# Kernel tuning notes

Hardware: AMD Instinct MI355X
Metric: run time of the kernel (lower is better)

Reference implementation:

```python
import jax, jax.numpy as jnp
import numpy as np

T, HID = 2048, 2048
H, KV, D = 16, 2, 256
ROT = 64  # head_dim * partial_rotary_factor (0.25)
THETA = 1.0e7
EPS = 1e-6
SCALE = D ** -0.5


def setup_inputs() -> dict:
    key = jax.random.key(0)
    ks = jax.random.split(key, 6)
    return {
        "positions": jnp.arange(T, dtype=jnp.int64 if jax.config.jax_enable_x64 else jnp.int32),
        "hidden_states": jax.random.normal(ks[0], (T, HID), jnp.float32),
        "wq": jax.random.normal(ks[1], (H * D * 2, HID), jnp.float32) * 0.02,
        "wk": jax.random.normal(ks[2], (KV * D, HID), jnp.float32) * 0.02,
        "wv": jax.random.normal(ks[3], (KV * D, HID), jnp.float32) * 0.02,
        "wo": jax.random.normal(ks[4], (HID, H * D), jnp.float32) * 0.02,
        "q_norm_w": jnp.zeros((D,), jnp.float32),
        "k_norm_w": jnp.zeros((D,), jnp.float32),
    }


def _rmsnorm(x, w):
    xf = x.astype(jnp.float32)
    out = xf * jax.lax.rsqrt(jnp.mean(xf * xf, axis=-1, keepdims=True) + EPS)
    return (out * (1.0 + w.astype(jnp.float32))).astype(x.dtype)


def _rope(positions, x):
    # partial rotary: first ROT dims, neox (rotate-half) style
    inv_freq = 1.0 / (THETA ** (jnp.arange(0, ROT, 2, dtype=jnp.float32) / ROT))
    freqs = positions.astype(jnp.float32)[:, None] * inv_freq  # [T, ROT/2]
    cos = jnp.cos(freqs)[:, None, :]  # [T,1,ROT/2]
    sin = jnp.sin(freqs)[:, None, :]
    x1 = x[..., : ROT // 2]
    x2 = x[..., ROT // 2 : ROT]
    rot = jnp.concatenate([x1 * cos - x2 * sin, x2 * cos + x1 * sin], axis=-1)
    return jnp.concatenate([rot, x[..., ROT:]], axis=-1)


def reference(positions, hidden_states, wq, wk, wv, wo, q_norm_w, k_norm_w):
    t = hidden_states.shape[0]
    q_out = (hidden_states @ wq.T).reshape(t, H, 2 * D)
    query, gate = q_out[..., :D], q_out[..., D:]
    gate = gate.reshape(t, H * D)
    k = (hidden_states @ wk.T).reshape(t, KV, D)
    v = (hidden_states @ wv.T).reshape(t, KV, D)

    query = _rmsnorm(query, q_norm_w)
    k = _rmsnorm(k, k_norm_w)
    query = _rope(positions, query)
    k = _rope(positions, k)

    # GQA: expand KV heads to H heads
    rep = H // KV
    k = jnp.repeat(k, rep, axis=1)  # [t, H, D]
    v = jnp.repeat(v, rep, axis=1)

    scores = jnp.einsum("qhd,khd->hqk", query, k) * SCALE
    causal = jnp.tril(jnp.ones((t, t), dtype=bool))
    scores = jnp.where(causal[None], scores, jnp.finfo(scores.dtype).min)
    probs = jax.nn.softmax(scores, axis=-1)
    o = jnp.einsum("hqk,khd->qhd", probs, v).reshape(t, H * D)

    o = o * jax.nn.sigmoid(gate)
    return o @ wo.T
```

## Files before the change

### kernel.cpp

```cpp
#include <hip/hip_runtime.h>
#include <hip/hip_bf16.h>

#define T_LEN 2048
#define HID_DIM 2048
#define NH 16
#define NKV 2
#define HD 256
#define ROT 64
#define EPS_F 1e-6f
#define SCALE_F 0.0625f
#define THETA_F 10000000.0f

typedef __bf16 bf16x8 __attribute__((ext_vector_type(8)));
typedef float floatx4 __attribute__((ext_vector_type(4)));

__device__ __forceinline__ unsigned short f2bf(float x) {
  unsigned int u = __float_as_uint(x);
  unsigned int rounding = 0x7FFFu + ((u >> 16) & 1u);
  return (unsigned short)((u + rounding) >> 16);
}
__device__ __forceinline__ float bf2f(unsigned short u) {
  return __uint_as_float(((unsigned int)u) << 16);
}
__device__ __forceinline__ floatx4 mfma16(bf16x8 a, bf16x8 b, floatx4 c) {
  return __builtin_amdgcn_mfma_f32_16x16x32_bf16(a, b, c, 0, 0, 0);
}
__device__ __forceinline__ void gl_lds16(const unsigned short* g, unsigned short* l) {
  __builtin_amdgcn_global_load_lds(
      (const __attribute__((address_space(1))) unsigned int*)g,
      (__attribute__((address_space(3))) unsigned int*)l, 16, 0, 0);
}

__global__ __launch_bounds__(256) void cvt_all(
    const float* __restrict__ hs, const float* __restrict__ wq,
    const float* __restrict__ wk, const float* __restrict__ wv,
    const float* __restrict__ wo, unsigned short* __restrict__ hsb,
    unsigned short* __restrict__ qkvwb, unsigned short* __restrict__ wob,
    const int* __restrict__ pos, float2* __restrict__ tab) {
  int i = blockIdx.x * 256 + threadIdx.x;
  if (i >= 7864320) {
    const int tid = i - 7864320;
    const int t = tid >> 5, fi = tid & 31;
    const float fr = (float)pos[t] * exp2f(-(float)fi * (23.2534966642f / 32.0f));
    tab[tid] = make_float2(cosf(fr), sinf(fr));
    return;
  }
  const float4* s4;
  ushort4* d4;
  int j;
  if (i < 1048576) { s4 = (const float4*)hs; d4 = (ushort4*)hsb; j = i; }
  else if (i < 5242880) { s4 = (const float4*)wq; d4 = (ushort4*)qkvwb; j = i - 1048576; }
  else if (i < 5505024) { s4 = (const float4*)wk; d4 = (ushort4*)qkvwb + 4194304; j = i - 5242880; }
  else if (i < 5767168) { s4 = (const float4*)wv; d4 = (ushort4*)qkvwb + 4456448; j = i - 5505024; }
  else { s4 = (const float4*)wo; d4 = (ushort4*)wob; j = i - 5767168; }
  float4 v = s4[j];
  ushort4 o;
  o.x = f2bf(v.x); o.y = f2bf(v.y); o.z = f2bf(v.z); o.w = f2bf(v.w);
  d4[j] = o;
}

__global__ __launch_bounds__(256) void gemm_bf16_bt(
    const unsigned short* __restrict__ A,
    const unsigned short* __restrict__ B,
    void* __restrict__ Cv, void* __restrict__ Cv2, int M, int N, int ld,
    int Ksub, int c_bf16, unsigned short* __restrict__ vTout) {
  __shared__ alignas(16) unsigned short As[2][128 * 32];
  __shared__ alignas(16) unsigned short Bs[2][128 * 32];
  const int tid = threadIdx.x;
  const int m0 = blockIdx.y * 128;
  const int n0 = blockIdx.x * 128;
  const int koff = blockIdx.z * Ksub;
  const int lane = tid & 63;
  const int wave = tid >> 6;
  const int wm = (wave >> 1) * 64;
  const int wn = (wave & 1) * 64;
  const int lrow = lane & 15;
  const int kgrp = lane >> 4;

  const unsigned short* aG = A + (size_t)(m0 + wave * 32 + (lane >> 2)) * ld + (lane & 3) * 8 + koff;
  const unsigned short* bG = B + (size_t)(n0 + wave * 32 + (lane >> 2)) * ld + (lane & 3) * 8 + koff;

  auto stage = [&](int k0, int b) {
    gl_lds16(aG + k0, &As[b][(wave * 32) * 32]);
    gl_lds16(aG + (size_t)16 * ld + k0, &As[b][(wave * 32 + 16) * 32]);
    gl_lds16(bG + k0, &Bs[b][(wave * 32) * 32]);
    gl_lds16(bG + (size_t)16 * ld + k0, &Bs[b][(wave * 32 + 16) * 32]);
  };

  floatx4 acc[4][4];
#pragma unroll
  for (int i = 0; i < 4; i++)
#pragma unroll
    for (int j = 0; j < 4; j++) acc[i][j] = floatx4{0.f, 0.f, 0.f, 0.f};

  stage(0, 0);
  __syncthreads();
  int cur = 0;
  for (int k0 = 0; k0 < Ksub; k0 += 32) {
    if (k0 + 32 < Ksub) stage(k0 + 32, cur ^ 1);
    bf16x8 af[4], bfr[4];
#pragma unroll
    for (int i = 0; i < 4; i++)
      af[i] = *reinterpret_cast<const bf16x8*>(&As[cur][(wm + i * 16 + lrow) * 32 + kgrp * 8]);
#pragma unroll
    for (int j = 0; j < 4; j++)
      bfr[j] = *reinterpret_cast<const bf16x8*>(&Bs[cur][(wn + j * 16 + lrow) * 32 + kgrp * 8]);
#pragma unroll
    for (int i = 0; i < 4; i++)
#pragma unroll
      for (int j = 0; j < 4; j++)
        acc[i][j] = mfma16(af[i], bfr[j], acc[i][j]);
    __syncthreads();
    cur ^= 1;
  }

  if (c_bf16) {
    unsigned short* C = (unsigned short*)Cv;
    const bool vtile = (vTout != nullptr) && (n0 >= 8704);
#pragma unroll
    for (int i = 0; i < 4; i++) {
      int row = m0 + wm + i * 16 + kgrp * 4;
#pragma unroll
      for (int j = 0; j < 4; j++) {
        int col = n0 + wn + j * 16 + lrow;
        if (vtile) {
          unsigned short* vrow = vTout + (size_t)(col - 8704) * T_LEN + row;
#pragma unroll
          for (int r = 0; r < 4; r++) vrow[r] = f2bf(acc[i][j][r]);
        } else {
#pragma unroll
          for (int r = 0; r < 4; r++)
            C[(size_t)(row + r) * N + col] = f2bf(acc[i][j][r]);
        }
      }
    }
  } else {
    float* base = (blockIdx.z < 2) ? (float*)Cv : (float*)Cv2;
    float* C = base + (size_t)(blockIdx.z & 1) * M * N;
#pragma unroll
    for (int i = 0; i < 4; i++) {
      int row = m0 + wm + i * 16 + kgrp * 4;
#pragma unroll
      for (int j = 0; j < 4; j++) {
        int col = n0 + wn + j * 16 + lrow;
#pragma unroll
        for (int r = 0; r < 4; r++)
          C[(size_t)(row + r) * N + col] = acc[i][j][r];
      }
    }
  }
}

__global__ __launch_bounds__(256) void add_out(
    const float* __restrict__ p0, const float* __restrict__ p1,
    float* __restrict__ out, int n4) {
  int i = blockIdx.x * 256 + threadIdx.x;
  if (i >= n4) return;
  float4 a = ((const float4*)p0)[i];
  float4 b = ((const float4*)p0)[i + n4];
  float4 c = ((const float4*)p1)[i];
  float4 d = ((const float4*)p1)[i + n4];
  float4 o;
  o.x = (a.x + b.x) + (c.x + d.x);
  o.y = (a.y + b.y) + (c.y + d.y);
  o.z = (a.z + b.z) + (c.z + d.z);
  o.w = (a.w + b.w) + (c.w + d.w);
  ((float4*)out)[i] = o;
}

__global__ __launch_bounds__(256) void norm_rope_fused(
    const unsigned short* __restrict__ qkv, const float* __restrict__ qw,
    const float* __restrict__ kw, const float2* __restrict__ tab,
    unsigned short* __restrict__ qbf, unsigned short* __restrict__ kbf) {
  const int t = blockIdx.x;
  const int y = blockIdx.y;
  const int wv = threadIdx.x >> 6;
  const int lane = threadIdx.x & 63;
  const unsigned short* in;
  const float* w;
  unsigned short* outp;
  if (y < 4) {
    const int h = y * 4 + wv;
    in = qkv + (size_t)t * 9216 + h * 512;
    w = qw;
    outp = qbf + (size_t)t * (NH * HD) + h * HD;
  } else {
    if (wv >= NKV) return;
    in = qkv + (size_t)t * 9216 + 8192 + wv * HD;
    w = kw;
    outp = kbf + (size_t)t * (NKV * HD) + wv * HD;
  }
  const int d0 = lane * 4;
  ushort4 v = *reinterpret_cast<const ushort4*>(in + d0);
  float x0 = bf2f(v.x), x1 = bf2f(v.y), x2 = bf2f(v.z), x3 = bf2f(v.w);
  float ss = (x0 * x0 + x1 * x1) + (x2 * x2 + x3 * x3);
#pragma unroll
  for (int m = 32; m >= 1; m >>= 1) ss += __shfl_xor(ss, m);
  const float rms = rsqrtf(ss * (1.0f / 256.0f) + EPS_F);
  float4 w4 = *reinterpret_cast<const float4*>(w + d0);
  float y0 = x0 * rms * (1.0f + w4.x);
  float y1 = x1 * rms * (1.0f + w4.y);
  float y2 = x2 * rms * (1.0f + w4.z);
  float y3 = x3 * rms * (1.0f + w4.w);
  if (lane < 16) {
    float p0 = __shfl_xor(y0, 8);
    float p1 = __shfl_xor(y1, 8);
    float p2 = __shfl_xor(y2, 8);
    float p3 = __shfl_xor(y3, 8);
    const float2* trow = tab + t * 32 + (d0 & 31);
    float4 cs01 = *reinterpret_cast<const float4*>(trow);
    float4 cs23 = *reinterpret_cast<const float4*>(trow + 2);
    if (d0 < 32) {
      y0 = y0 * cs01.x - p0 * cs01.y;
      y1 = y1 * cs01.z - p1 * cs01.w;
      y2 = y2 * cs23.x - p2 * cs23.y;
      y3 = y3 * cs23.z - p3 * cs23.w;
    } else {
      y0 = p0 * cs01.y + y0 * cs01.x;
      y1 = p1 * cs01.w + y1 * cs01.z;
      y2 = p2 * cs23.y + y2 * cs23.x;
      y3 = p3 * cs23.w + y3 * cs23.z;
    }
  }
  ushort4 ov;
  ov.x = f2bf(y0); ov.y = f2bf(y1); ov.z = f2bf(y2); ov.w = f2bf(y3);
  *reinterpret_cast<ushort4*>(outp + d0) = ov;
}

__global__ __launch_bounds__(256, 2) void attn_fwd(
    const unsigned short* __restrict__ qbf,
    const unsigned short* __restrict__ kbf,
    const unsigned short* __restrict__ vT,
    const unsigned short* __restrict__ qkvout,
    unsigned short* __restrict__ og)
{
  const int t = 31 - (int)blockIdx.x;
  const int h = blockIdx.y;
  const int wv = threadIdx.x >> 6;
  const int lane = threadIdx.x & 63;
  const int lrow = lane & 15;
  const int kgrp = lane >> 4;
  const int kv = h >> 3;
  const int q0 = t * 64 + wv * 16;
  const int nb = t * 2 + 2;

  __shared__ alignas(16) unsigned short Ks[32 * 256];
  __shared__ alignas(16) unsigned short Vs[2][256 * 32];
  __shared__ alignas(16) unsigned short Ps[4][16 * 32];

  auto stage_k = [&](int kb) {
#pragma unroll
    for (int i = 0; i < 4; ++i) {
      const int inst = wv * 4 + i;
      const int key_loc = inst * 2 + (lane >> 5);
      const int c = (lane & 31) ^ (key_loc & 7);
      const unsigned short* g =
          kbf + (size_t)(kb + key_loc) * (NKV * HD) + kv * HD + c * 8;
      gl_lds16(g, &Ks[inst * 512]);
    }
  };
  auto stage_v = [&](int kb, int buf) {
#pragma unroll
    for (int i = 0; i < 4; ++i) {
      const int inst = wv * 4 + i;
      const int dim = inst * 16 + (lane >> 2);
      const int c = (lane & 3) ^ (dim & 3);
      const unsigned short* g =
          vT + (size_t)(kv * HD + dim) * T_LEN + kb + c * 8;
      gl_lds16(g, &Vs[buf][inst * 512]);
    }
  };

  bf16x8 qa[8];
  {
    const unsigned short* qr = qbf + (size_t)(q0 + lrow) * (NH * HD) + h * HD + kgrp * 8;
#pragma unroll
    for (int s = 0; s < 8; s++)
      qa[s] = *reinterpret_cast<const bf16x8*>(qr + s * 32);
  }

  float lp[4] = {0.f, 0.f, 0.f, 0.f};
  floatx4 o[16];
#pragma unroll
  for (int dt = 0; dt < 16; dt++) o[dt] = floatx4{0.f, 0.f, 0.f, 0.f};

  stage_k(0);
  stage_v(0, 0);

  for (int ib = 0; ib < nb; ++ib) {
    const int kb = ib * 32;
    __syncthreads();
    if (ib + 1 < nb) stage_v(kb + 32, (ib + 1) & 1);

    const bool d = kb <= q0 + 15;

    floatx4 s0[2];
#pragma unroll
    for (int j = 0; j < 2; j++) s0[j] = floatx4{0.f, 0.f, 0.f, 0.f};
#pragma unroll
    for (int j = 0; j < 2; ++j) {
      const int ks = kb + j * 16;
      if (!(d && (ks <= q0 + 15))) continue;
      bf16x8 kf[8];
#pragma unroll
      for (int s = 0; s < 8; s++)
        kf[s] = *reinterpret_cast<const bf16x8*>(
            &Ks[(j * 16 + lrow) * 256 + (((s * 4 + kgrp) ^ (lrow & 7)) * 8)]);
#pragma unroll
      for (int s = 0; s < 8; s++) s0[j] = mfma16(qa[s], kf[s], s0[j]);
    }

    if (d) {
#pragma unroll
      for (int r = 0; r < 4; ++r) {
        const int qr = q0 + kgrp * 4 + r;
        float p0 = (kb + lrow <= qr) ? __expf(s0[0][r] * SCALE_F) : 0.f;
        float p1 = (kb + 16 + lrow <= qr) ? __expf(s0[1][r] * SCALE_F) : 0.f;
        lp[r] += p0 + p1;
        Ps[wv][(kgrp * 4 + r) * 32 + lrow] = f2bf(p0);
        Ps[wv][(kgrp * 4 + r) * 32 + 16 + lrow] = f2bf(p1);
      }
    }

    __syncthreads();
    if (ib + 1 < nb) stage_k(kb + 32);

    if (d) {
      bf16x8 pa = *reinterpret_cast<const bf16x8*>(&Ps[wv][lrow * 32 + kgrp * 8]);
      const unsigned short* vsb = &Vs[ib & 1][0];
#pragma unroll
      for (int dt = 0; dt < 16; ++dt) {
        const int dd = dt * 16 + lrow;
        bf16x8 bv = *reinterpret_cast<const bf16x8*>(
            &vsb[dd * 32 + ((kgrp ^ (lrow & 3)) * 8)]);
        o[dt] = mfma16(pa, bv, o[dt]);
      }
    }
  }

#pragma unroll
  for (int r = 0; r < 4; ++r) {
#pragma unroll
    for (int m = 8; m >= 1; m >>= 1) lp[r] += __shfl_xor(lp[r], m);
  }

#pragma unroll
  for (int r = 0; r < 4; ++r) {
    const int row = q0 + kgrp * 4 + r;
    const float inv_l = 1.0f / lp[r];
    const unsigned short* grow = qkvout + (size_t)row * 9216 + h * 512 + 256;
    unsigned short* orow = og + (size_t)row * (NH * HD) + h * HD;
#pragma unroll
    for (int dt = 0; dt < 16; dt++) {
      int dim = dt * 16 + lrow;
      float g = bf2f(grow[dim]);
      float val = o[dt][r] * inv_l;
      val *= 1.0f / (1.0f + __expf(-g));
      orow[dim] = f2bf(val);
    }
  }
}

extern "C" void kernel_launch(void* const* d_in, const int* in_sizes, int n_in,
                              void* d_out, int out_size, void* d_ws, size_t ws_size,
                              hipStream_t stream) {
  const int* positions = (const int*)d_in[0];
  const float* hidden = (const float*)d_in[1];
  const float* wq = (const float*)d_in[2];
  const float* wk = (const float*)d_in[3];
  const float* wv = (const float*)d_in[4];
  const float* wo = (const float*)d_in[5];
  const float* qnw = (const float*)d_in[6];
  const float* knw = (const float*)d_in[7];
  float* out = (float*)d_out;

  char* ws = (char*)d_ws;
  size_t off = 0;
  auto alloc = [&](size_t elems) -> unsigned short* {
    unsigned short* p = (unsigned short*)(ws + off);
    off += (elems * 2 + 255) & ~(size_t)255;
    return p;
  };
  unsigned short* hsb    = alloc((size_t)T_LEN * HID_DIM);
  unsigned short* qkvwb  = alloc((size_t)9216 * HID_DIM);
  unsigned short* wob    = alloc((size_t)HID_DIM * NH * HD);
  unsigned short* qkvout = alloc((size_t)T_LEN * 9216);
  unsigned short* qbf    = alloc((size_t)T_LEN * NH * HD);
  unsigned short* kbf    = alloc((size_t)T_LEN * NKV * HD);
  unsigned short* vTb    = alloc((size_t)NKV * HD * T_LEN);
  unsigned short* og     = alloc((size_t)T_LEN * NH * HD);
  float2* ropetab = (float2*)alloc((size_t)T_LEN * 32 * 4);
  float* part01 = (float*)ws;
  float* part23 = (float*)qkvout;

  cvt_all<<<30976, 256, 0, stream>>>(hidden, wq, wk, wv, wo, hsb, qkvwb, wob,
                                     positions, ropetab);

  gemm_bf16_bt<<<dim3(72, 16, 1), 256, 0, stream>>>(hsb, qkvwb, qkvout, nullptr,
                                                    2048, 9216, 2048, 2048, 1, vTb);

  norm_rope_fused<<<dim3(T_LEN, 5), 256, 0, stream>>>(qkvout, qnw, knw, ropetab, qbf, kbf);

  attn_fwd<<<dim3(32, NH), 256, 0, stream>>>(qbf, kbf, vTb, qkvout, og);

  gemm_bf16_bt<<<dim3(16, 16, 4), 256, 0, stream>>>(og, wob, part01, part23,
                                                    2048, 2048, 4096, 1024, 0, nullptr);
  add_out<<<4096, 256, 0, stream>>>(part01, part23, out, 1048576);
}
```

Measured before the change: 439.7 us.

## Fuse Q norm and RoPE into attention prologue and halve output split-K

Query RMSNorm and partial RoPE are now applied inside the attention kernel directly from the QKV GEMM output, so the separate q buffer write/read disappears and the norm kernel only handles K. The output projection uses split-K of 2 instead of 4, shrinking the partial-sum traffic and simplifying the final reduction. K/V staging is issued before the Q prologue to overlap its latency. The trade-off is extra per-thread ALU work in attention and fewer blocks in the output GEMM.

```diff
diff --git a/kernel.cpp b/kernel.cpp
--- a/kernel.cpp
+++ b/kernel.cpp
@@ -152,44 +152,24 @@
 }
 
 __global__ __launch_bounds__(256) void add_out(
-    const float* __restrict__ p0, const float* __restrict__ p1,
-    float* __restrict__ out, int n4) {
+    const float* __restrict__ p, float* __restrict__ out, int n4) {
   int i = blockIdx.x * 256 + threadIdx.x;
   if (i >= n4) return;
-  float4 a = ((const float4*)p0)[i];
-  float4 b = ((const float4*)p0)[i + n4];
-  float4 c = ((const float4*)p1)[i];
-  float4 d = ((const float4*)p1)[i + n4];
+  float4 a = ((const float4*)p)[i];
+  float4 b = ((const float4*)p)[i + n4];
   float4 o;
-  o.x = (a.x + b.x) + (c.x + d.x);
-  o.y = (a.y + b.y) + (c.y + d.y);
-  o.z = (a.z + b.z) + (c.z + d.z);
-  o.w = (a.w + b.w) + (c.w + d.w);
+  o.x = a.x + b.x; o.y = a.y + b.y; o.z = a.z + b.z; o.w = a.w + b.w;
   ((float4*)out)[i] = o;
 }
 
-__global__ __launch_bounds__(256) void norm_rope_fused(
-    const unsigned short* __restrict__ qkv, const float* __restrict__ qw,
-    const float* __restrict__ kw, const float2* __restrict__ tab,
-    unsigned short* __restrict__ qbf, unsigned short* __restrict__ kbf) {
+__global__ __launch_bounds__(128) void norm_rope_k(
+    const unsigned short* __restrict__ qkv, const float* __restrict__ kw,
+    const float2* __restrict__ tab, unsigned short* __restrict__ kbf) {
   const int t = blockIdx.x;
-  const int y = blockIdx.y;
   const int wv = threadIdx.x >> 6;
   const int lane = threadIdx.x & 63;
-  const unsigned short* in;
-  const float* w;
-  unsigned short* outp;
-  if (y < 4) {
-    const int h = y * 4 + wv;
-    in = qkv + (size_t)t * 9216 + h * 512;
-    w = qw;
-    outp = qbf + (size_t)t * (NH * HD) + h * HD;
-  } else {
-    if (wv >= NKV) return;
-    in = qkv + (size_t)t * 9216 + 8192 + wv * HD;
-    w = kw;
-    outp = kbf + (size_t)t * (NKV * HD) + wv * HD;
-  }
+  const unsigned short* in = qkv + (size_t)t * 9216 + 8192 + wv * HD;
+  unsigned short* outp = kbf + (size_t)t * (NKV * HD) + wv * HD;
   const int d0 = lane * 4;
   ushort4 v = *reinterpret_cast<const ushort4*>(in + d0);
   float x0 = bf2f(v.x), x1 = bf2f(v.y), x2 = bf2f(v.z), x3 = bf2f(v.w);
@@ -197,7 +177,7 @@
 #pragma unroll
   for (int m = 32; m >= 1; m >>= 1) ss += __shfl_xor(ss, m);
   const float rms = rsqrtf(ss * (1.0f / 256.0f) + EPS_F);
-  float4 w4 = *reinterpret_cast<const float4*>(w + d0);
+  float4 w4 = *reinterpret_cast<const float4*>(kw + d0);
   float y0 = x0 * rms * (1.0f + w4.x);
   float y1 = x1 * rms * (1.0f + w4.y);
   float y2 = x2 * rms * (1.0f + w4.z);
@@ -228,10 +208,11 @@
 }
 
 __global__ __launch_bounds__(256, 2) void attn_fwd(
-    const unsigned short* __restrict__ qbf,
+    const unsigned short* __restrict__ qkvout,
     const unsigned short* __restrict__ kbf,
     const unsigned short* __restrict__ vT,
-    const unsigned short* __restrict__ qkvout,
+    const float* __restrict__ qw,
+    const float2* __restrict__ tab,
     unsigned short* __restrict__ og)
 {
   const int t = 31 - (int)blockIdx.x;
@@ -271,21 +252,45 @@
     }
   };
 
+  stage_k(0);
+  stage_v(0, 0);
+
   bf16x8 qa[8];
   {
-    const unsigned short* qr = qbf + (size_t)(q0 + lrow) * (NH * HD) + h * HD + kgrp * 8;
+    const unsigned short* qr = qkvout + (size_t)(q0 + lrow) * 9216 + h * 512 + kgrp * 8;
 #pragma unroll
     for (int s = 0; s < 8; s++)
       qa[s] = *reinterpret_cast<const bf16x8*>(qr + s * 32);
+    unsigned short* qe = reinterpret_cast<unsigned short*>(qa);
+    float ss = 0.f;
+#pragma unroll
+    for (int e = 0; e < 64; e++) { float x = bf2f(qe[e]); ss += x * x; }
+    ss += __shfl_xor(ss, 16);
+    ss += __shfl_xor(ss, 32);
+    const float rms = rsqrtf(ss * (1.0f / 256.0f) + EPS_F);
+    const float2* trow = tab + (size_t)(q0 + lrow) * 32;
+#pragma unroll
+    for (int j = 0; j < 8; j++) {
+      const int dlo = kgrp * 8 + j;
+      float ylo = bf2f(qe[j]) * rms * (1.0f + qw[dlo]);
+      float yhi = bf2f(qe[8 + j]) * rms * (1.0f + qw[dlo + 32]);
+      float2 cs = trow[dlo];
+      qe[j] = f2bf(ylo * cs.x - yhi * cs.y);
+      qe[8 + j] = f2bf(yhi * cs.x + ylo * cs.y);
+    }
+#pragma unroll
+    for (int s = 2; s < 8; s++)
+#pragma unroll
+      for (int j = 0; j < 8; j++) {
+        const int d = kgrp * 8 + s * 32 + j;
+        qe[s * 8 + j] = f2bf(bf2f(qe[s * 8 + j]) * rms * (1.0f + qw[d]));
+      }
   }
 
   float lp[4] = {0.f, 0.f, 0.f, 0.f};
   floatx4 o[16];
 #pragma unroll
   for (int dt = 0; dt < 16; dt++) o[dt] = floatx4{0.f, 0.f, 0.f, 0.f};
-
-  stage_k(0);
-  stage_v(0, 0);
 
   for (int ib = 0; ib < nb; ++ib) {
     const int kb = ib * 32;
@@ -385,13 +390,11 @@
   unsigned short* qkvwb  = alloc((size_t)9216 * HID_DIM);
   unsigned short* wob    = alloc((size_t)HID_DIM * NH * HD);
   unsigned short* qkvout = alloc((size_t)T_LEN * 9216);
-  unsigned short* qbf    = alloc((size_t)T_LEN * NH * HD);
   unsigned short* kbf    = alloc((size_t)T_LEN * NKV * HD);
   unsigned short* vTb    = alloc((size_t)NKV * HD * T_LEN);
   unsigned short* og     = alloc((size_t)T_LEN * NH * HD);
   float2* ropetab = (float2*)alloc((size_t)T_LEN * 32 * 4);
-  float* part01 = (float*)ws;
-  float* part23 = (float*)qkvout;
+  float* part = (float*)ws;
 
   cvt_all<<<30976, 256, 0, stream>>>(hidden, wq, wk, wv, wo, hsb, qkvwb, wob,
                                      positions, ropetab);
@@ -399,11 +402,11 @@
   gemm_bf16_bt<<<dim3(72, 16, 1), 256, 0, stream>>>(hsb, qkvwb, qkvout, nullptr,
                                                     2048, 9216, 2048, 2048, 1, vTb);
 
-  norm_rope_fused<<<dim3(T_LEN, 5), 256, 0, stream>>>(qkvout, qnw, knw, ropetab, qbf, kbf);
-
-  attn_fwd<<<dim3(32, NH), 256, 0, stream>>>(qbf, kbf, vTb, qkvout, og);
-
-  gemm_bf16_bt<<<dim3(16, 16, 4), 256, 0, stream>>>(og, wob, part01, part23,
-                                                    2048, 2048, 4096, 1024, 0, nullptr);
-  add_out<<<4096, 256, 0, stream>>>(part01, part23, out, 1048576);
-}
+  norm_rope_k<<<T_LEN, 128, 0, stream>>>(qkvout, knw, ropetab, kbf);
+
+  attn_fwd<<<dim3(32, NH), 256, 0, stream>>>(qkvout, kbf, vTb, qnw, ropetab, og);
+
+  gemm_bf16_bt<<<dim3(16, 16, 2), 256, 0, stream>>>(og, wob, part, nullptr,
+                                                    2048, 2048, 4096, 2048, 0, nullptr);
+  add_out<<<4096, 256, 0, stream>>>(part, out, 1048576);
+}
```

After: 430.1 us. -2.2%, faster.
